# Performance work log

Hardware: AMD Instinct MI355X
Metric: run time of the kernel (lower is better)

The kernel has to match this reference:

```python
import jax, jax.numpy as jnp
import numpy as np

B, S, D, H = 2, 2048, 1024, 16
HD = D // H          # 64
NREF = HD // 2       # 32 Householder reflections
BLOCK = 128          # flex_attention block granularity
ROPE_BASE = 10000.0


def setup_inputs() -> dict:
    key = jax.random.key(0)
    ks = jax.random.split(key, 12)
    x = jax.random.normal(ks[0], (B, S, D), jnp.float32)
    # block-causal block mask (flex_attention block_mask analogue)
    nb = S // BLOCK
    bm = jnp.tril(jnp.ones((nb, nb), bool))
    mask = jnp.repeat(jnp.repeat(bm, BLOCK, axis=0), BLOCK, axis=1)  # [S,S]
    s = lambda fan: fan ** -0.5
    vs = jax.random.normal(ks[1], (NREF, HD), jnp.float32) * 0.02
    w_qkv = jax.random.normal(ks[2], (D, 3 * D), jnp.float32) * s(D)
    w_out = jax.random.normal(ks[3], (D, D), jnp.float32) * s(D)
    w_gate = jax.random.normal(ks[4], (D, D), jnp.float32) * s(D)
    b_gate = jnp.zeros((D,), jnp.float32)
    w_mlp_gate = jax.random.normal(ks[5], (D, 8 * D), jnp.float32) * s(D)
    b_mlp_gate = jnp.zeros((8 * D,), jnp.float32)
    w_mlp_out = jax.random.normal(ks[6], (4 * D, D), jnp.float32) * s(4 * D)
    b_mlp_out = jnp.zeros((D,), jnp.float32)
    return dict(x=x, mask=mask, grid_size=S, vs=vs, w_qkv=w_qkv, w_out=w_out,
                w_gate=w_gate, b_gate=b_gate, w_mlp_gate=w_mlp_gate,
                b_mlp_gate=b_mlp_gate, w_mlp_out=w_mlp_out, b_mlp_out=b_mlp_out)


def rmsnorm(x):
    return x * jax.lax.rsqrt(jnp.mean(x * x, axis=-1, keepdims=True) + 1e-6)


def householder_matrix(vs):
    # Q = prod_i (I - 2 v_i v_i^T / |v_i|^2), applied sequentially as in torch loop
    def body(Q, v):
        vn = jnp.sum(v * v) + 1e-8
        return Q - (2.0 / vn) * jnp.outer(v, v @ Q), None
    Q0 = jnp.eye(HD, dtype=vs.dtype)
    Q, _ = jax.lax.scan(body, Q0, vs)
    return Q


def rope_tables(seq_len, dtype):
    inv_freq = 1.0 / (ROPE_BASE ** (jnp.arange(0, HD, 2, dtype=jnp.float32) / HD))
    ang = jnp.arange(seq_len, dtype=jnp.float32)[:, None] * inv_freq  # [S, HD/2]
    ang = jnp.concatenate([ang, ang], axis=-1)                        # [S, HD]
    return jnp.cos(ang).astype(dtype), jnp.sin(ang).astype(dtype)


def rotate_half(x):
    x1, x2 = jnp.split(x, 2, axis=-1)
    return jnp.concatenate([-x2, x1], axis=-1)


def reference(x, mask, grid_size, vs, w_qkv, w_out, w_gate, b_gate,
              w_mlp_gate, b_mlp_gate, w_mlp_out, b_mlp_out):
    del grid_size  # positions derived from sequence length
    resid = x
    h = rmsnorm(x)
    qkv = h @ w_qkv                                # [B,S,3D]
    q, k, v = jnp.split(qkv, 3, axis=-1)
    to_heads = lambda t: t.reshape(B, S, H, HD).transpose(0, 2, 1, 3)  # [B,H,S,hd]
    q, k, v = to_heads(q), to_heads(k), to_heads(v)

    # RnRoPE: inverse Householder rotation, rope, forward Householder rotation
    Q = householder_matrix(vs)                     # [hd,hd]
    q = q @ Q.T
    k = k @ Q.T
    cos, sin = rope_tables(S, x.dtype)             # [S,hd]
    cos = cos[None, None]; sin = sin[None, None]
    q = q * cos + rotate_half(q) * sin
    k = k * cos + rotate_half(k) * sin
    q = q @ Q
    k = k @ Q

    # block-sparse attention (mask realized as boolean [S,S])
    scores = jnp.einsum('bhqd,bhkd->bhqk', q, k) / jnp.sqrt(jnp.asarray(HD, x.dtype))
    scores = jnp.where(mask[None, None], scores, jnp.asarray(-1e30, x.dtype))
    attn = jnp.einsum('bhqk,bhkd->bhqd', jax.nn.softmax(scores, axis=-1), v)
    attn = attn.transpose(0, 2, 1, 3).reshape(B, S, D)
    attn = attn @ w_out

    gate = jax.nn.sigmoid(attn @ w_gate + b_gate)
    x = resid + attn * gate

    resid = x
    gv = rmsnorm(x) @ w_mlp_gate + b_mlp_gate      # [B,S,8D]
    g, val = jnp.split(gv, 2, axis=-1)
    x = resid + (val * jax.nn.gelu(g, approximate=False)) @ w_mlp_out + b_mlp_out
    return x
```

## Files before the change

kernel.cpp:

```cpp
#include <hip/hip_runtime.h>
#include <hip/hip_bf16.h>
#include <math.h>

#define BT 2
#define SEQ 2048
#define DIM 1024
#define NH 16
#define HD 64
#define NTOK (BT*SEQ)

typedef __attribute__((ext_vector_type(4))) float floatx4;
typedef __attribute__((ext_vector_type(8))) short shortx8;
typedef __attribute__((ext_vector_type(4))) short shortx4;

#define GLL16(gp, lp) __builtin_amdgcn_global_load_lds( \
    (const __attribute__((address_space(1))) unsigned int*)(const void*)(gp), \
    (__attribute__((address_space(3))) unsigned int*)(void*)(lp), 16, 0, 0)

__device__ __forceinline__ float bf2f(unsigned short u) {
    unsigned int x = ((unsigned int)u) << 16;
    return __builtin_bit_cast(float, x);
}
__device__ __forceinline__ unsigned short f2bf(float f) {
    unsigned int x = __builtin_bit_cast(unsigned int, f);
    unsigned int lsb = (x >> 16) & 1u;
    x += 0x7fffu + lsb;
    return (unsigned short)(x >> 16);
}
__device__ __forceinline__ float ldin_f(const void* p, size_t i, int isbf) {
    return isbf ? bf2f(((const unsigned short*)p)[i]) : ((const float*)p)[i];
}

__global__ void detect_kernel(const unsigned short* __restrict__ x, int* __restrict__ flag) {
    __shared__ int cnt;
    if (threadIdx.x == 0) cnt = 0;
    __syncthreads();
    unsigned short u = x[(size_t)threadIdx.x * 2];
    int e = (u >> 7) & 0xFF;
    if (e >= 100 && e <= 140) atomicAdd(&cnt, 1);
    __syncthreads();
    if (threadIdx.x == 0) *flag = (cnt >= 192) ? 1 : 0;
}

__global__ void transpose_any(const void* __restrict__ in,
                              unsigned short* __restrict__ out, int R, int C,
                              const int* __restrict__ flagp) {
    int isbf = *flagp;
    __shared__ unsigned short tile[32][33];
    int c0 = blockIdx.x * 32, r0 = blockIdx.y * 32;
    int tx = threadIdx.x, ty = threadIdx.y;
#pragma unroll
    for (int i = 0; i < 4; i++) {
        size_t idx = (size_t)(r0 + ty + i * 8) * C + c0 + tx;
        tile[ty + i * 8][tx] = isbf ? ((const unsigned short*)in)[idx]
                                    : f2bf(((const float*)in)[idx]);
    }
    __syncthreads();
#pragma unroll
    for (int i = 0; i < 4; i++)
        out[(size_t)(c0 + ty + i * 8) * R + r0 + tx] = tile[tx][ty + i * 8];
}

__global__ __launch_bounds__(64) void householder_kernel(const void* __restrict__ vs,
                                                         float* __restrict__ Qg,
                                                         const int* __restrict__ flagp) {
    int isbf = *flagp;
    __shared__ float vsh[64];
    int j = threadIdx.x;
    float Qc[64];
#pragma unroll
    for (int i = 0; i < 64; i++) Qc[i] = (i == j) ? 1.f : 0.f;
    for (int r = 0; r < 32; r++) {
        vsh[j] = ldin_f(vs, r * 64 + j, isbf);
        __syncthreads();
        float va[64];
#pragma unroll
        for (int i = 0; i < 64; i++) va[i] = vsh[i];
        float vn0 = 0.f, vn1 = 0.f, vn2 = 0.f, vn3 = 0.f;
        float t0 = 0.f, t1 = 0.f, t2 = 0.f, t3 = 0.f;
#pragma unroll
        for (int i = 0; i < 16; i++) {
            vn0 += va[4 * i + 0] * va[4 * i + 0];
            vn1 += va[4 * i + 1] * va[4 * i + 1];
            vn2 += va[4 * i + 2] * va[4 * i + 2];
            vn3 += va[4 * i + 3] * va[4 * i + 3];
            t0 += va[4 * i + 0] * Qc[4 * i + 0];
            t1 += va[4 * i + 1] * Qc[4 * i + 1];
            t2 += va[4 * i + 2] * Qc[4 * i + 2];
            t3 += va[4 * i + 3] * Qc[4 * i + 3];
        }
        float vn = (vn0 + vn1) + (vn2 + vn3) + 1e-8f;
        float t = (t0 + t1) + (t2 + t3);
        float c = (2.f / vn) * t;
#pragma unroll
        for (int i = 0; i < 64; i++) Qc[i] -= c * va[i];
        __syncthreads();
    }
#pragma unroll
    for (int i = 0; i < 64; i++) Qg[i * 64 + j] = Qc[i];
}

__global__ __launch_bounds__(256) void rotate_wqkv(unsigned short* __restrict__ wT,
                                                   const float* __restrict__ Qg) {
    __shared__ float Qs[64][64];
    __shared__ unsigned short tile[64][128];
    int bid = blockIdx.x;
    int row0 = (bid >> 3) * 64;
    int col0 = (bid & 7) * 128;
    int t = threadIdx.x;
#pragma unroll
    for (int i = 0; i < 16; i++) {
        int idx = i * 256 + t;
        Qs[idx >> 6][idx & 63] = Qg[idx];
    }
#pragma unroll
    for (int i = 0; i < 8; i++) {
        int e = i * 256 + t;
        int r = e >> 5, cg = (e & 31) * 4;
        *(shortx4*)&tile[r][cg] = *(const shortx4*)&wT[(size_t)(row0 + r) * 1024 + col0 + cg];
    }
    __syncthreads();
    int ib = t >> 5;
    int c = (t & 31) * 4;
    float acc[8][4];
#pragma unroll
    for (int rr = 0; rr < 8; rr++)
#pragma unroll
        for (int cx = 0; cx < 4; cx++) acc[rr][cx] = 0.f;
    for (int j = 0; j < 64; j++) {
        float t0 = bf2f(tile[j][c]);
        float t1 = bf2f(tile[j][c + 1]);
        float t2 = bf2f(tile[j][c + 2]);
        float t3 = bf2f(tile[j][c + 3]);
#pragma unroll
        for (int rr = 0; rr < 8; rr++) {
            float qv = Qs[rr * 8 + ib][j];
            acc[rr][0] += qv * t0;
            acc[rr][1] += qv * t1;
            acc[rr][2] += qv * t2;
            acc[rr][3] += qv * t3;
        }
    }
#pragma unroll
    for (int rr = 0; rr < 8; rr++) {
        int i = rr * 8 + ib;
        shortx4 o4;
#pragma unroll
        for (int cx = 0; cx < 4; cx++) o4[cx] = (short)f2bf(acc[rr][cx]);
        *(shortx4*)&wT[(size_t)(row0 + i) * 1024 + col0 + c] = o4;
    }
}

__global__ void rope_table(float* __restrict__ tab) {
    int idx = blockIdx.x * 256 + threadIdx.x;
    int s = idx >> 5, fi = idx & 31;
    float invf = __expf(-(float)fi * (9.210340371976184f / 32.f));
    float ang = (float)s * invf;
    tab[2 * idx]     = cosf(ang);
    tab[2 * idx + 1] = sinf(ang);
}

__global__ __launch_bounds__(256) void rmsnorm2(const void* __restrict__ x,
                                                unsigned short* __restrict__ h,
                                                const int* __restrict__ flagp) {
    int isbf = flagp ? *flagp : 1;
    __shared__ float red[256];
    int row = blockIdx.x, t = threadIdx.x;
    size_t base = (size_t)row * DIM;
    float v[4];
    float ss = 0.f;
#pragma unroll
    for (int i = 0; i < 4; i++) {
        v[i] = ldin_f(x, base + t + 256 * i, isbf);
        ss += v[i] * v[i];
    }
    red[t] = ss;
    __syncthreads();
    for (int s = 128; s > 0; s >>= 1) {
        if (t < s) red[t] += red[t + s];
        __syncthreads();
    }
    float rs = rsqrtf(red[0] * (1.f / 1024.f) + 1e-6f);
#pragma unroll
    for (int i = 0; i < 4; i++) h[base + t + 256 * i] = f2bf(v[i] * rs);
}

template<int BN>
__global__ __launch_bounds__(256) void gemm_bt(const unsigned short* __restrict__ A,
                                               const unsigned short* __restrict__ Bt,
                                               void* __restrict__ C,
                                               const void* __restrict__ bias,
                                               const unsigned short* __restrict__ resid,
                                               const int* __restrict__ flagp,
                                               int M, int N, int K, int c_f32) {
    constexpr int NJ = BN / 32;
    __shared__ __align__(16) unsigned short As[128][32];
    __shared__ __align__(16) unsigned short Bs[BN][32];
    int bisbf = (bias && flagp) ? *flagp : 1;
    int tile = (blockIdx.x & 7) * (gridDim.x >> 3) + (blockIdx.x >> 3);
    int nbn = N / BN;
    int m0 = (tile / nbn) * 128;
    int n0 = (tile % nbn) * BN;
    int t = threadIdx.x;
    int lane = t & 63;
    int w = t >> 6;
    int wr = (w >> 1) * 64;
    int wc = (w & 1) * (16 * NJ);
    int lr = lane & 15;
    int kg = lane >> 4;

    floatx4 acc[4][NJ];
#pragma unroll
    for (int i = 0; i < 4; i++)
#pragma unroll
        for (int j = 0; j < NJ; j++) acc[i][j] = (floatx4){0.f, 0.f, 0.f, 0.f};

    int srow = w * 16 + (lane >> 2);
    int skseg = (lane & 3) * 8;
    const unsigned short* aP = A + (size_t)(m0 + srow) * K + skseg;
    const unsigned short* bP = Bt + (size_t)(n0 + srow) * K + skseg;
    unsigned short* aL0 = &As[w * 16][0];
    unsigned short* aL1 = &As[64 + w * 16][0];
    unsigned short* bL0 = &Bs[w * 16][0];
    size_t r64 = (size_t)64 * K;

    for (int k0 = 0; k0 < K; k0 += 32) {
        __syncthreads();
        GLL16(aP + k0,       aL0);
        GLL16(aP + r64 + k0, aL1);
        GLL16(bP + k0,       bL0);
        if constexpr (BN == 128) {
            unsigned short* bL1 = &Bs[(BN == 128 ? 64 : 0) + w * 16][0];
            GLL16(bP + r64 + k0, bL1);
        }
        __syncthreads();
        shortx8 af[4], bfv[NJ];
#pragma unroll
        for (int i = 0; i < 4; i++) af[i] = *(const shortx8*)&As[wr + i * 16 + lr][kg * 8];
#pragma unroll
        for (int j = 0; j < NJ; j++) bfv[j] = *(const shortx8*)&Bs[wc + j * 16 + lr][kg * 8];
#pragma unroll
        for (int i = 0; i < 4; i++)
#pragma unroll
            for (int j = 0; j < NJ; j++)
                acc[i][j] = __builtin_amdgcn_mfma_f32_16x16x32_bf16(af[i], bfv[j], acc[i][j], 0, 0, 0);
    }
#pragma unroll
    for (int i = 0; i < 4; i++) {
#pragma unroll
        for (int j = 0; j < NJ; j++) {
            int col = n0 + wc + j * 16 + lr;
            int rbase = m0 + wr + i * 16 + kg * 4;
            float bv = bias ? ldin_f(bias, col, bisbf) : 0.f;
#pragma unroll
            for (int r = 0; r < 4; r++) {
                float val = acc[i][j][r] + bv;
                size_t oidx = (size_t)(rbase + r) * N + col;
                if (resid) val += bf2f(resid[oidx]);
                if (c_f32) ((float*)C)[oidx] = val;
                else       ((unsigned short*)C)[oidx] = f2bf(val);
            }
        }
    }
}

__global__ __launch_bounds__(256) void gemm_glu(const unsigned short* __restrict__ A,
                                                const unsigned short* __restrict__ Bt,
                                                unsigned short* __restrict__ act,
                                                const void* __restrict__ bias,
                                                const int* __restrict__ flagp) {
    __shared__ __align__(16) unsigned short As[128][32];
    __shared__ __align__(16) unsigned short Bg[64][32];
    __shared__ __align__(16) unsigned short Bv[64][32];
    const int K = 1024;
    int isbf = *flagp;
    int tile = (blockIdx.x & 7) * (gridDim.x >> 3) + (blockIdx.x >> 3);
    int m0 = (tile >> 6) * 128;
    int n0 = (tile & 63) * 64;
    int t = threadIdx.x;
    int lane = t & 63;
    int w = t >> 6;
    int wr = (w >> 1) * 64;
    int wc = (w & 1) * 32;
    int lr = lane & 15;
    int kg = lane >> 4;

    floatx4 ag[4][2], av[4][2];
#pragma unroll
    for (int i = 0; i < 4; i++)
#pragma unroll
        for (int j = 0; j < 2; j++) {
            ag[i][j] = (floatx4){0.f, 0.f, 0.f, 0.f};
            av[i][j] = (floatx4){0.f, 0.f, 0.f, 0.f};
        }

    int srow = w * 16 + (lane >> 2);
    int skseg = (lane & 3) * 8;
    const unsigned short* aP  = A + (size_t)(m0 + srow) * K + skseg;
    const unsigned short* bgP = Bt + (size_t)(n0 + srow) * K + skseg;
    const unsigned short* bvP = Bt + (size_t)(4096 + n0 + srow) * K + skseg;
    unsigned short* aL0 = &As[w * 16][0];
    unsigned short* aL1 = &As[64 + w * 16][0];
    unsigned short* gL  = &Bg[w * 16][0];
    unsigned short* vL  = &Bv[w * 16][0];
    size_t r64 = (size_t)64 * K;

    for (int k0 = 0; k0 < K; k0 += 32) {
        __syncthreads();
        GLL16(aP + k0,       aL0);
        GLL16(aP + r64 + k0, aL1);
        GLL16(bgP + k0,      gL);
        GLL16(bvP + k0,      vL);
        __syncthreads();
        shortx8 af[4], gf[2], vf[2];
#pragma unroll
        for (int i = 0; i < 4; i++) af[i] = *(const shortx8*)&As[wr + i * 16 + lr][kg * 8];
#pragma unroll
        for (int j = 0; j < 2; j++) {
            gf[j] = *(const shortx8*)&Bg[wc + j * 16 + lr][kg * 8];
            vf[j] = *(const shortx8*)&Bv[wc + j * 16 + lr][kg * 8];
        }
#pragma unroll
        for (int i = 0; i < 4; i++)
#pragma unroll
            for (int j = 0; j < 2; j++) {
                ag[i][j] = __builtin_amdgcn_mfma_f32_16x16x32_bf16(af[i], gf[j], ag[i][j], 0, 0, 0);
                av[i][j] = __builtin_amdgcn_mfma_f32_16x16x32_bf16(af[i], vf[j], av[i][j], 0, 0, 0);
            }
    }
#pragma unroll
    for (int i = 0; i < 4; i++) {
#pragma unroll
        for (int j = 0; j < 2; j++) {
            int col = n0 + wc + j * 16 + lr;
            int rbase = m0 + wr + i * 16 + kg * 4;
            float bgv = ldin_f(bias, col, isbf);
            float bvv = ldin_f(bias, 4096 + col, isbf);
#pragma unroll
            for (int r = 0; r < 4; r++) {
                float g = ag[i][j][r] + bgv;
                float v = av[i][j][r] + bvv;
                float ge = 0.5f * g * (1.f + erff(g * 0.70710678118f));
                act[(size_t)(rbase + r) * 4096 + col] = f2bf(v * ge);
            }
        }
    }
}

__global__ __launch_bounds__(256) void qk_rope3(const unsigned short* __restrict__ qkv,
                                                const float* __restrict__ tab,
                                                unsigned short* __restrict__ q_r,
                                                unsigned short* __restrict__ k_r) {
    int tid = blockIdx.x * 256 + threadIdx.x;
    int c = tid & 3;
    int h = (tid >> 2) & 15;
    int ts = tid >> 6;
    int s = ts & 2047, b = ts >> 11;
    int d0 = c * 8;
    const unsigned short* base = qkv + (size_t)ts * 3072 + h * 64;
    shortx8 qlo = *(const shortx8*)(base + d0);
    shortx8 qhi = *(const shortx8*)(base + d0 + 32);
    shortx8 klo = *(const shortx8*)(base + 1024 + d0);
    shortx8 khi = *(const shortx8*)(base + 1024 + d0 + 32);
    const float* tp = tab + (size_t)s * 64 + d0 * 2;
    shortx8 oql, oqh, okl, okh;
#pragma unroll
    for (int i = 0; i < 8; i++) {
        float cv = tp[2 * i], sv = tp[2 * i + 1];
        float ql = bf2f((unsigned short)qlo[i]), qh = bf2f((unsigned short)qhi[i]);
        float kl = bf2f((unsigned short)klo[i]), kh = bf2f((unsigned short)khi[i]);
        oql[i] = (short)f2bf(ql * cv - qh * sv);
        oqh[i] = (short)f2bf(qh * cv + ql * sv);
        okl[i] = (short)f2bf(kl * cv - kh * sv);
        okh[i] = (short)f2bf(kh * cv + kl * sv);
    }
    size_t o = ((size_t)(b * NH + h) * SEQ + s) * HD + d0;
    *(shortx8*)(q_r + o)      = oql;
    *(shortx8*)(q_r + o + 32) = oqh;
    *(shortx8*)(k_r + o)      = okl;
    *(shortx8*)(k_r + o + 32) = okh;
}

__global__ __launch_bounds__(512) void attn_mfma(const unsigned short* __restrict__ q_r,
                                                 const unsigned short* __restrict__ k_r,
                                                 const unsigned short* __restrict__ qkv,
                                                 unsigned short* __restrict__ attn) {
    __shared__ __align__(16) unsigned short Ks[64][72];
    __shared__ __align__(16) unsigned short Vt[64 * 72];
    __shared__ __align__(16) unsigned short Ps[8][16][72];
    int bid = blockIdx.x;
    int qblk = 15 - (bid & 15);
    int bh = bid >> 4;
    int b = bh >> 4, h = bh & 15;
    size_t bh_off = (size_t)bh * SEQ * HD;
    int tid = threadIdx.x;
    int wv = tid >> 6, lane = tid & 63;
    int l16 = lane & 15, quad = lane >> 4;
    int q0 = qblk * 128 + wv * 16;

    const unsigned short* qrow = q_r + bh_off + (size_t)(q0 + l16) * HD + quad * 8;
    shortx8 aq0 = *(const shortx8*)(qrow);
    shortx8 aq1 = *(const shortx8*)(qrow + 32);

    floatx4 o[4];
#pragma unroll
    for (int nt = 0; nt < 4; nt++) o[nt] = (floatx4){0.f, 0.f, 0.f, 0.f};
    float m_run = -1e30f, l_run = 0.f;

    int nk = (qblk + 1) * 128;
    int skey = tid >> 3;
    int sd0 = (tid & 7) * 8;
    const unsigned short* kbase = k_r + bh_off + (size_t)skey * HD + sd0;
    const unsigned short* vbase = qkv + ((size_t)(b * SEQ + skey)) * 3072 + 2048 + h * 64 + sd0;
    int vco = (((skey >> 3) ^ (tid & 7)) * 8) + (skey & 7);

    shortx8 kv = *(const shortx8*)kbase;
    shortx8 vvv = *(const shortx8*)vbase;

    for (int k0 = 0; k0 < nk; k0 += 64) {
        __syncthreads();
        *(shortx8*)&Ks[skey][sd0] = kv;
#pragma unroll
        for (int i = 0; i < 8; i++) Vt[(size_t)(sd0 + i) * 72 + vco] = (unsigned short)vvv[i];
        __syncthreads();
        if (k0 + 64 < nk) {
            kv  = *(const shortx8*)(kbase + (size_t)(k0 + 64) * HD);
            vvv = *(const shortx8*)(vbase + (size_t)(k0 + 64) * 3072);
        }

        floatx4 sc[4];
#pragma unroll
        for (int kt = 0; kt < 4; kt++) {
            shortx8 bk0 = *(const shortx8*)&Ks[kt * 16 + l16][quad * 8];
            shortx8 bk1 = *(const shortx8*)&Ks[kt * 16 + l16][32 + quad * 8];
            floatx4 z = (floatx4){0.f, 0.f, 0.f, 0.f};
            z = __builtin_amdgcn_mfma_f32_16x16x32_bf16(bk0, aq0, z, 0, 0, 0);
            z = __builtin_amdgcn_mfma_f32_16x16x32_bf16(bk1, aq1, z, 0, 0, 0);
            sc[kt] = z;
        }
        float sv[16], mx[16];
#pragma unroll
        for (int kt = 0; kt < 4; kt++)
#pragma unroll
            for (int r = 0; r < 4; r++) sv[kt * 4 + r] = sc[kt][r] * 0.125f;
#pragma unroll
        for (int i = 0; i < 16; i++) mx[i] = sv[i];
#pragma unroll
        for (int st = 8; st > 0; st >>= 1)
#pragma unroll
            for (int i = 0; i < 8; i++)
                if (i < st) mx[i] = fmaxf(mx[i], mx[i + st]);
        float mt = mx[0];
        mt = fmaxf(mt, __shfl_xor(mt, 16, 64));
        mt = fmaxf(mt, __shfl_xor(mt, 32, 64));
        float nm = fmaxf(m_run, mt);
        float al = __expf(m_run - nm);
        m_run = nm;
        float p[16];
#pragma unroll
        for (int i = 0; i < 16; i++) p[i] = __expf(sv[i] - nm);
        float sm[8];
#pragma unroll
        for (int i = 0; i < 8; i++) sm[i] = p[i] + p[i + 8];
        float ps = ((sm[0] + sm[1]) + (sm[2] + sm[3])) + ((sm[4] + sm[5]) + (sm[6] + sm[7]));
        ps += __shfl_xor(ps, 16, 64);
        ps += __shfl_xor(ps, 32, 64);
        l_run = l_run * al + ps;
#pragma unroll
        for (int kt = 0; kt < 4; kt++) {
            shortx4 pk;
#pragma unroll
            for (int r = 0; r < 4; r++) pk[r] = (short)f2bf(p[kt * 4 + r]);
            *(shortx4*)&Ps[wv][l16][kt * 16 + quad * 4] = pk;
        }
#pragma unroll
        for (int r = 0; r < 4; r++) {
            float alr = __shfl(al, quad * 4 + r, 64);
            o[0][r] *= alr; o[1][r] *= alr; o[2][r] *= alr; o[3][r] *= alr;
        }
#pragma unroll
        for (int h2 = 0; h2 < 2; h2++) {
            shortx8 ap = *(const shortx8*)&Ps[wv][l16][h2 * 32 + quad * 8];
#pragma unroll
            for (int nt = 0; nt < 4; nt++) {
                int dd = nt * 16 + l16;
                shortx8 bvv = *(const shortx8*)&Vt[(size_t)dd * 72 +
                                                   (((h2 * 4 + quad) ^ ((dd >> 3) & 7)) * 8)];
                o[nt] = __builtin_amdgcn_mfma_f32_16x16x32_bf16(ap, bvv, o[nt], 0, 0, 0);
            }
        }
    }
#pragma unroll
    for (int r = 0; r < 4; r++) {
        float lv = __shfl(l_run, quad * 4 + r, 64);
        float inv_l = 1.f / lv;
        int s = q0 + quad * 4 + r;
        unsigned short* op = attn + ((size_t)(b * SEQ + s)) * DIM + h * 64;
#pragma unroll
        for (int nt = 0; nt < 4; nt++) op[nt * 16 + l16] = f2bf(o[nt][r] * inv_l);
    }
}

__global__ void combine_gate(const void* __restrict__ x,
                             const unsigned short* __restrict__ ao,
                             const unsigned short* __restrict__ gl,
                             const void* __restrict__ bg,
                             unsigned short* __restrict__ x1,
                             const int* __restrict__ flagp) {
    int isbf = *flagp;
    size_t idx = (size_t)blockIdx.x * 256 + threadIdx.x;
    float a = bf2f(ao[idx]);
    float z = bf2f(gl[idx]) + ldin_f(bg, idx & 1023, isbf);
    float sg = 1.f / (1.f + __expf(-z));
    x1[idx] = f2bf(ldin_f(x, idx, isbf) + a * sg);
}

extern "C" void kernel_launch(void* const* d_in, const int* in_sizes, int n_in,
                              void* d_out, int out_size, void* d_ws, size_t ws_size,
                              hipStream_t stream) {
    const unsigned short* x        = (const unsigned short*)d_in[0];
    const void* vs       = d_in[3];
    const void* w_qkv    = d_in[4];
    const void* w_out    = d_in[5];
    const void* w_gate   = d_in[6];
    const void* b_gate   = d_in[7];
    const void* w_mlp_g  = d_in[8];
    const void* b_mlp_g  = d_in[9];
    const void* w_mlp_o  = d_in[10];
    const void* b_mlp_o  = d_in[11];
    float* out = (float*)d_out;
    char* ws = (char*)d_ws;

    if (n_in < 12) return;
    if (in_sizes[0] != 4194304 || in_sizes[3] != 2048 || in_sizes[4] != 3145728 ||
        in_sizes[8] != 8388608 || in_sizes[10] != 4194304 || in_sizes[7] != 1024) return;

    const size_t o_T   = 0;
    const size_t o_Qg  = 35651584;
    const size_t o_h   = 35684352;
    const size_t o_B   = 44072960;
    const size_t o_C   = 69238784;
    const size_t o_gv  = 94404608;
    const size_t total = 161513472;
    if (ws_size < total) return;

    unsigned short* wqkvT  = (unsigned short*)(ws + o_T);
    unsigned short* woutT  = (unsigned short*)(ws + o_T + 6291456);
    unsigned short* wgateT = (unsigned short*)(ws + o_T + 8388608);
    unsigned short* wmgT   = (unsigned short*)(ws + o_T + 10485760);
    unsigned short* wmoT   = (unsigned short*)(ws + o_T + 27262976);
    float*          Qg     = (float*)(ws + o_Qg);
    int*            flagp  = (int*)(ws + o_Qg + 16384);
    unsigned short* h      = (unsigned short*)(ws + o_h);
    unsigned short* qkv    = (unsigned short*)(ws + o_B);
    unsigned short* ao     = (unsigned short*)(ws + o_B + 8388608);
    unsigned short* gl     = (unsigned short*)(ws + o_B + 16777216);
    unsigned short* q_rb   = (unsigned short*)(ws + o_C);
    unsigned short* k_rb   = (unsigned short*)(ws + o_C + 8388608);
    unsigned short* attnb  = (unsigned short*)(ws + o_C + 16777216);
    unsigned short* x1     = (unsigned short*)(ws + o_C);
    unsigned short* act    = (unsigned short*)(ws + o_C + 8388608);
    float*          rtab   = (float*)(ws + o_gv);

    detect_kernel<<<1, 256, 0, stream>>>(x, flagp);
    householder_kernel<<<1, 64, 0, stream>>>(vs, Qg, flagp);
    rope_table<<<256, 256, 0, stream>>>(rtab);

    dim3 tb(32, 8);
    transpose_any<<<dim3(3072 / 32, 1024 / 32), tb, 0, stream>>>(w_qkv,   wqkvT, 1024, 3072, flagp);
    transpose_any<<<dim3(1024 / 32, 1024 / 32), tb, 0, stream>>>(w_out,   woutT, 1024, 1024, flagp);
    transpose_any<<<dim3(1024 / 32, 1024 / 32), tb, 0, stream>>>(w_gate,  wgateT, 1024, 1024, flagp);
    transpose_any<<<dim3(8192 / 32, 1024 / 32), tb, 0, stream>>>(w_mlp_g, wmgT, 1024, 8192, flagp);
    transpose_any<<<dim3(1024 / 32, 4096 / 32), tb, 0, stream>>>(w_mlp_o, wmoT, 4096, 1024, flagp);
    rotate_wqkv<<<256, 256, 0, stream>>>(wqkvT, Qg);

    rmsnorm2<<<NTOK, 256, 0, stream>>>(x, h, flagp);
    gemm_bt<128><<<32 * 24, 256, 0, stream>>>(h, wqkvT, qkv, nullptr, nullptr, flagp, NTOK, 3072, 1024, 0);
    qk_rope3<<<1024, 256, 0, stream>>>(qkv, rtab, q_rb, k_rb);
    attn_mfma<<<BT * NH * (SEQ / 128), 512, 0, stream>>>(q_rb, k_rb, qkv, attnb);
    gemm_bt<64><<<32 * 16, 256, 0, stream>>>(attnb, woutT, ao, nullptr, nullptr, flagp, NTOK, 1024, 1024, 0);
    gemm_bt<64><<<32 * 16, 256, 0, stream>>>(ao, wgateT, gl, nullptr, nullptr, flagp, NTOK, 1024, 1024, 0);
    combine_gate<<<NTOK * DIM / 256, 256, 0, stream>>>(x, ao, gl, b_gate, x1, flagp);
    rmsnorm2<<<NTOK, 256, 0, stream>>>(x1, h, nullptr);
    gemm_glu<<<32 * 64, 256, 0, stream>>>(h, wmgT, act, b_mlp_g, flagp);
    gemm_bt<64><<<32 * 16, 256, 0, stream>>>(act, wmoT, (void*)out, b_mlp_o, x1, flagp, NTOK, 1024, 4096, 1);
}
```

Measured before the change: 583.2 us.

## Double-buffer LDS tiles in GEMM kernels and reorder GLU tile mapping

Both the generic GEMM and the GLU GEMM now keep two LDS buffers and prefetch the next K-slice via global_load_lds while MFMAs run on the current one, dropping one barrier per iteration. The goal is to hide global-memory latency behind compute. The GLU kernel also changes its tile index mapping so consecutive tiles walk M first, which alters L2 reuse of weight versus activation tiles. LDS use doubles, which may lower occupancy, and the single barrier relies on the compiler's vmcnt waits being placed correctly before the next read.

```diff
diff --git a/kernel.cpp b/kernel.cpp
--- a/kernel.cpp
+++ b/kernel.cpp
@@ -194,8 +194,8 @@
                                                const int* __restrict__ flagp,
                                                int M, int N, int K, int c_f32) {
     constexpr int NJ = BN / 32;
-    __shared__ __align__(16) unsigned short As[128][32];
-    __shared__ __align__(16) unsigned short Bs[BN][32];
+    __shared__ __align__(16) unsigned short As[2][128][32];
+    __shared__ __align__(16) unsigned short Bs[2][BN][32];
     int bisbf = (bias && flagp) ? *flagp : 1;
     int tile = (blockIdx.x & 7) * (gridDim.x >> 3) + (blockIdx.x >> 3);
     int nbn = N / BN;
@@ -219,31 +219,35 @@
     int skseg = (lane & 3) * 8;
     const unsigned short* aP = A + (size_t)(m0 + srow) * K + skseg;
     const unsigned short* bP = Bt + (size_t)(n0 + srow) * K + skseg;
-    unsigned short* aL0 = &As[w * 16][0];
-    unsigned short* aL1 = &As[64 + w * 16][0];
-    unsigned short* bL0 = &Bs[w * 16][0];
     size_t r64 = (size_t)64 * K;
 
+    GLL16(aP,       &As[0][w * 16][0]);
+    GLL16(aP + r64, &As[0][64 + w * 16][0]);
+    GLL16(bP,       &Bs[0][w * 16][0]);
+    if constexpr (BN == 128) GLL16(bP + r64, &Bs[0][64 + w * 16][0]);
+    __syncthreads();
+
+    int cur = 0;
     for (int k0 = 0; k0 < K; k0 += 32) {
-        __syncthreads();
-        GLL16(aP + k0,       aL0);
-        GLL16(aP + r64 + k0, aL1);
-        GLL16(bP + k0,       bL0);
-        if constexpr (BN == 128) {
-            unsigned short* bL1 = &Bs[(BN == 128 ? 64 : 0) + w * 16][0];
-            GLL16(bP + r64 + k0, bL1);
-        }
-        __syncthreads();
+        if (k0 + 32 < K) {
+            int nb = cur ^ 1;
+            GLL16(aP + k0 + 32,       &As[nb][w * 16][0]);
+            GLL16(aP + r64 + k0 + 32, &As[nb][64 + w * 16][0]);
+            GLL16(bP + k0 + 32,       &Bs[nb][w * 16][0]);
+            if constexpr (BN == 128) GLL16(bP + r64 + k0 + 32, &Bs[nb][64 + w * 16][0]);
+        }
         shortx8 af[4], bfv[NJ];
 #pragma unroll
-        for (int i = 0; i < 4; i++) af[i] = *(const shortx8*)&As[wr + i * 16 + lr][kg * 8];
-#pragma unroll
-        for (int j = 0; j < NJ; j++) bfv[j] = *(const shortx8*)&Bs[wc + j * 16 + lr][kg * 8];
+        for (int i = 0; i < 4; i++) af[i] = *(const shortx8*)&As[cur][wr + i * 16 + lr][kg * 8];
+#pragma unroll
+        for (int j = 0; j < NJ; j++) bfv[j] = *(const shortx8*)&Bs[cur][wc + j * 16 + lr][kg * 8];
 #pragma unroll
         for (int i = 0; i < 4; i++)
 #pragma unroll
             for (int j = 0; j < NJ; j++)
                 acc[i][j] = __builtin_amdgcn_mfma_f32_16x16x32_bf16(af[i], bfv[j], acc[i][j], 0, 0, 0);
+        __syncthreads();
+        cur ^= 1;
     }
 #pragma unroll
     for (int i = 0; i < 4; i++) {
@@ -269,14 +273,14 @@
                                                 unsigned short* __restrict__ act,
                                                 const void* __restrict__ bias,
                                                 const int* __restrict__ flagp) {
-    __shared__ __align__(16) unsigned short As[128][32];
-    __shared__ __align__(16) unsigned short Bg[64][32];
-    __shared__ __align__(16) unsigned short Bv[64][32];
+    __shared__ __align__(16) unsigned short As[2][128][32];
+    __shared__ __align__(16) unsigned short Bg[2][64][32];
+    __shared__ __align__(16) unsigned short Bv[2][64][32];
     const int K = 1024;
     int isbf = *flagp;
     int tile = (blockIdx.x & 7) * (gridDim.x >> 3) + (blockIdx.x >> 3);
-    int m0 = (tile >> 6) * 128;
-    int n0 = (tile & 63) * 64;
+    int m0 = (tile & 31) * 128;
+    int n0 = (tile >> 5) * 64;
     int t = threadIdx.x;
     int lane = t & 63;
     int w = t >> 6;
@@ -299,26 +303,30 @@
     const unsigned short* aP  = A + (size_t)(m0 + srow) * K + skseg;
     const unsigned short* bgP = Bt + (size_t)(n0 + srow) * K + skseg;
     const unsigned short* bvP = Bt + (size_t)(4096 + n0 + srow) * K + skseg;
-    unsigned short* aL0 = &As[w * 16][0];
-    unsigned short* aL1 = &As[64 + w * 16][0];
-    unsigned short* gL  = &Bg[w * 16][0];
-    unsigned short* vL  = &Bv[w * 16][0];
     size_t r64 = (size_t)64 * K;
 
+    GLL16(aP,       &As[0][w * 16][0]);
+    GLL16(aP + r64, &As[0][64 + w * 16][0]);
+    GLL16(bgP,      &Bg[0][w * 16][0]);
+    GLL16(bvP,      &Bv[0][w * 16][0]);
+    __syncthreads();
+
+    int cur = 0;
     for (int k0 = 0; k0 < K; k0 += 32) {
-        __syncthreads();
-        GLL16(aP + k0,       aL0);
-        GLL16(aP + r64 + k0, aL1);
-        GLL16(bgP + k0,      gL);
-        GLL16(bvP + k0,      vL);
-        __syncthreads();
+        if (k0 + 32 < K) {
+            int nb = cur ^ 1;
+            GLL16(aP + k0 + 32,       &As[nb][w * 16][0]);
+            GLL16(aP + r64 + k0 + 32, &As[nb][64 + w * 16][0]);
+            GLL16(bgP + k0 + 32,      &Bg[nb][w * 16][0]);
+            GLL16(bvP + k0 + 32,      &Bv[nb][w * 16][0]);
+        }
         shortx8 af[4], gf[2], vf[2];
 #pragma unroll
-        for (int i = 0; i < 4; i++) af[i] = *(const shortx8*)&As[wr + i * 16 + lr][kg * 8];
+        for (int i = 0; i < 4; i++) af[i] = *(const shortx8*)&As[cur][wr + i * 16 + lr][kg * 8];
 #pragma unroll
         for (int j = 0; j < 2; j++) {
-            gf[j] = *(const shortx8*)&Bg[wc + j * 16 + lr][kg * 8];
-            vf[j] = *(const shortx8*)&Bv[wc + j * 16 + lr][kg * 8];
+            gf[j] = *(const shortx8*)&Bg[cur][wc + j * 16 + lr][kg * 8];
+            vf[j] = *(const shortx8*)&Bv[cur][wc + j * 16 + lr][kg * 8];
         }
 #pragma unroll
         for (int i = 0; i < 4; i++)
@@ -327,6 +335,8 @@
                 ag[i][j] = __builtin_amdgcn_mfma_f32_16x16x32_bf16(af[i], gf[j], ag[i][j], 0, 0, 0);
                 av[i][j] = __builtin_amdgcn_mfma_f32_16x16x32_bf16(af[i], vf[j], av[i][j], 0, 0, 0);
             }
+        __syncthreads();
+        cur ^= 1;
     }
 #pragma unroll
     for (int i = 0; i < 4; i++) {
```

Measured after the change: 576.8 us. Within noise of the previous version (-1.1%).
